# Kernel tuning notes

Hardware: AMD Instinct MI355X
Metric: run time of the kernel (lower is better)

The kernel has to match this reference:

```python
import jax, jax.numpy as jnp
import numpy as np

K = 2
N_NODES = 100_000
N_EDGES = 1_600_000
STATIC_F = 16
DYN_F = 32
EDGE_F = 8
IN_F = EDGE_F + 2 * STATIC_F + 2 * DYN_F  # 104
HID_F = 2 * DYN_F  # 64


def setup_inputs() -> dict:
    key = jax.random.key(0)
    ks = jax.random.split(key, 9)
    x_s = jax.random.normal(ks[0], (N_NODES, STATIC_F), dtype=jnp.float32)
    x_t = jax.random.normal(ks[1], (N_NODES, DYN_F), dtype=jnp.float32)
    edge_index = jax.random.randint(ks[2], (2, N_EDGES), 0, N_NODES, dtype=jnp.int64 if jax.config.jax_enable_x64 else jnp.int32)
    edge_attr = jax.random.normal(ks[3], (N_EDGES, EDGE_F), dtype=jnp.float32)
    W1 = jax.random.normal(ks[4], (IN_F, HID_F), dtype=jnp.float32) / np.sqrt(IN_F)
    b1 = jnp.zeros((HID_F,), dtype=jnp.float32)
    W2 = jax.random.normal(ks[5], (HID_F, DYN_F), dtype=jnp.float32) / np.sqrt(HID_F)
    b2 = jnp.zeros((DYN_F,), dtype=jnp.float32)
    F = jax.random.normal(ks[6], (K + 1, DYN_F, DYN_F), dtype=jnp.float32) / np.sqrt(DYN_F)
    return {"x_s": x_s, "x_t": x_t, "edge_index": edge_index, "edge_attr": edge_attr,
            "W1": W1, "b1": b1, "W2": W2, "b2": b2, "F": F}


def reference(x_s, x_t, edge_index, edge_attr, W1, b1, W2, b2, F):
    row, col = edge_index[0], edge_index[1]
    num_nodes = x_t.shape[0]
    # filter_matrix[0] (Linear, no bias); F[k] stored as [in, out]
    out = x_t @ F[0]
    xs_row = x_s[row]  # static gathers are loop-invariant
    xs_col = x_s[col]
    for k in range(K):
        mask = jnp.sum(out, axis=1) != 0  # [N]
        edge_mask = (mask[row] | mask[col]).astype(out.dtype)[:, None]  # [E,1]
        out_row = out[row]
        out_col = out[col]
        e_ij = jnp.concatenate([xs_row, xs_col, out_row, out_col, edge_attr], axis=1)  # [E,104]
        w_ij = jax.nn.relu(e_ij @ W1 + b1) @ W2 + b2  # [E,32]
        # normalize per edge; NaN (zero-norm) -> 0, matching masked_fill_
        nrm = jnp.linalg.norm(w_ij, axis=1, keepdims=True)
        w_ij = jnp.where(nrm > 0, w_ij / jnp.where(nrm > 0, nrm, 1.0), 0.0)
        # with_gradient: (x_j - x_i) * w_ij; zero out edges failing the mask
        shift = (out_col - out_row) * w_ij * edge_mask
        scattered = jax.ops.segment_sum(shift, col, num_segments=num_nodes)
        out = out + scattered @ F[k + 1]
    return out
```

## Files before the change

kernel.cpp:

```cpp
#include <hip/hip_runtime.h>

#define NN 100000
#define NE 1600000
#define SF 16
#define DF 32
#define EFT 8
#define HF 64

typedef __attribute__((ext_vector_type(8))) _Float16 half8;
typedef __attribute__((ext_vector_type(4))) _Float16 half4;
typedef __attribute__((ext_vector_type(8))) short short8;
typedef __attribute__((ext_vector_type(4))) float floatx4;

__global__ __launch_bounds__(256) void hist_kernel(const int* __restrict__ ei,
                                                   int* __restrict__ deg) {
  int e = blockIdx.x * 256 + threadIdx.x;
  if (e < NE) atomicAdd(&deg[ei[NE + e]], 1);
}

__global__ __launch_bounds__(256) void scan1_kernel(const int* __restrict__ deg,
                                                    int* __restrict__ cur,
                                                    int* __restrict__ bsums) {
  __shared__ int ts[256];
  int tid = threadIdx.x;
  int base = blockIdx.x * 1024 + tid * 4;
  int v[4];
#pragma unroll
  for (int q = 0; q < 4; ++q) v[q] = (base + q < NN) ? deg[base + q] : 0;
  int s = v[0] + v[1] + v[2] + v[3];
  ts[tid] = s;
  __syncthreads();
  for (int off = 1; off < 256; off <<= 1) {
    int t = (tid >= off) ? ts[tid - off] : 0;
    __syncthreads();
    ts[tid] += t;
    __syncthreads();
  }
  int excl = ts[tid] - s;
  if (tid == 255) bsums[blockIdx.x] = ts[255];
  int run = excl;
#pragma unroll
  for (int q = 0; q < 4; ++q) {
    if (base + q < NN) cur[base + q] = run;
    run += v[q];
  }
}

__global__ __launch_bounds__(256) void scan3_kernel(int* __restrict__ cur,
                                                    const int* __restrict__ bsums) {
  int i = blockIdx.x * 256 + threadIdx.x;
  int g = blockIdx.x >> 2;
  int pref = 0;
  for (int q = 0; q < g; ++q) pref += bsums[q];
  if (i < NN) cur[i] += pref;
}

__global__ __launch_bounds__(256) void setup_kernel(
    const float* __restrict__ W1, const float* __restrict__ W2,
    _Float16* __restrict__ WpreT, _Float16* __restrict__ w2pk,
    _Float16* __restrict__ w1epk,
    float4* __restrict__ scattered4, int* __restrict__ deg) {
  int gid = blockIdx.x * 256 + threadIdx.x;
  if (gid < 800000) {
    float4 z = {0.f, 0.f, 0.f, 0.f};
    scattered4[gid] = z;
  }
  if (gid < NN) deg[gid] = 0;
  if (gid < 128 * 64) {
    int col = gid >> 6, k = gid & 63;
    int j = col & 63;
    bool bh = col >= 64;
    float v = 0.f;
    if (k < 16) v = W1[((bh ? 16 : 0) + k) * HF + j];
    else if (k < 48) v = W1[((bh ? 64 : 32) + (k - 16)) * HF + j];
    WpreT[gid] = (_Float16)v;
  }
  if (gid < 2048) {
    int lane = gid >> 5, idx = gid & 31;
    int kt = idx >> 4, nt = (idx >> 3) & 1, q = idx & 7;
    int kgrp = (lane >> 4) & 3, lcol = lane & 15;
    w2pk[gid] = (_Float16)W2[(kt * 32 + kgrp * 8 + q) * DF + nt * 16 + lcol];
  } else if (gid < 4096) {
    int id = gid - 2048;
    int lane = id >> 5, idx = id & 31;
    int nt = idx >> 3, j = idx & 7;
    int lcol = lane & 15;
    float v = (lane < 16) ? W1[(96 + j) * HF + nt * 16 + lcol] : 0.f;
    w1epk[id] = (_Float16)v;
  }
}

__global__ __launch_bounds__(256) void fill_kernel(
    const int* __restrict__ ei, const float* __restrict__ ea,
    int* __restrict__ cur, int* __restrict__ row_s, int* __restrict__ col_s,
    _Float16* __restrict__ ea_s) {
  int e = blockIdx.x * 256 + threadIdx.x;
  int r = ei[e];
  int c = ei[NE + e];
  int pos = atomicAdd(&cur[c], 1);
  row_s[pos] = r;
  col_s[pos] = c;
  const float4* p = (const float4*)(ea + (size_t)e * EFT);
  float4 v0 = p[0], v1 = p[1];
  half8 h;
  h[0]=(_Float16)v0.x; h[1]=(_Float16)v0.y; h[2]=(_Float16)v0.z; h[3]=(_Float16)v0.w;
  h[4]=(_Float16)v1.x; h[5]=(_Float16)v1.y; h[6]=(_Float16)v1.z; h[7]=(_Float16)v1.w;
  *(half8*)(ea_s + (size_t)pos * 8) = h;
}

__global__ __launch_bounds__(256) void init_kernel(
    const float* __restrict__ x_t, const float* __restrict__ F0,
    float* __restrict__ out, _Float16* __restrict__ outb,
    float* __restrict__ sums) {
  int n = blockIdx.x * 256 + threadIdx.x;
  if (n >= NN) return;
  float x[DF];
  const float4* xr = reinterpret_cast<const float4*>(x_t + (size_t)n * DF);
#pragma unroll
  for (int q = 0; q < 8; ++q) {
    float4 v = xr[q];
    x[4*q+0]=v.x; x[4*q+1]=v.y; x[4*q+2]=v.z; x[4*q+3]=v.w;
  }
  float4* orow = reinterpret_cast<float4*>(out + (size_t)n * DF);
  _Float16* ob = outb + (size_t)n * DF;
  float s = 0.f;
#pragma unroll
  for (int q = 0; q < 8; ++q) {
    float4 acc = {0.f, 0.f, 0.f, 0.f};
#pragma unroll
    for (int i = 0; i < DF; ++i) {
      float xi = x[i];
      acc.x = fmaf(xi, F0[i*DF + 4*q+0], acc.x);
      acc.y = fmaf(xi, F0[i*DF + 4*q+1], acc.y);
      acc.z = fmaf(xi, F0[i*DF + 4*q+2], acc.z);
      acc.w = fmaf(xi, F0[i*DF + 4*q+3], acc.w);
    }
    orow[q] = acc;
    s += acc.x + acc.y + acc.z + acc.w;
    half4 pk = {(_Float16)acc.x, (_Float16)acc.y, (_Float16)acc.z, (_Float16)acc.w};
    *(half4*)(ob + 4*q) = pk;
  }
  sums[n] = s;
}

__global__ __launch_bounds__(256, 4) void pre_kernel(
    const float* __restrict__ x_s, const _Float16* __restrict__ outb,
    const _Float16* __restrict__ WpreT, _Float16* __restrict__ ABh) {
  __shared__ _Float16 wlds[128][72];
  int tid = threadIdx.x;
  for (int t = tid; t < 1024; t += 256) {
    int colr = t >> 3, kc = t & 7;
    *(half8*)(&wlds[colr][kc * 8]) = *(const half8*)(WpreT + colr * 64 + kc * 8);
  }
  __syncthreads();

  int lcol = tid & 15, kgrp = (tid >> 4) & 3, wid = tid >> 6;
  int nodebase = blockIdx.x * 64 + wid * 16;
  int nodeA = nodebase + lcol;

  half8 a0 = {}, a1 = {};
  if (nodeA < NN) {
    const _Float16* obp = outb + (size_t)nodeA * DF;
    if (kgrp < 2) {
      const float4* p = (const float4*)(x_s + (size_t)nodeA * SF);
      float4 v0 = p[kgrp * 2], v1 = p[kgrp * 2 + 1];
      a0[0]=(_Float16)v0.x; a0[1]=(_Float16)v0.y;
      a0[2]=(_Float16)v0.z; a0[3]=(_Float16)v0.w;
      a0[4]=(_Float16)v1.x; a0[5]=(_Float16)v1.y;
      a0[6]=(_Float16)v1.z; a0[7]=(_Float16)v1.w;
      a1 = *(const half8*)(obp + 16 + kgrp * 8);
    } else if (kgrp == 2) {
      a0 = *(const half8*)(obp + 0);
    } else {
      a0 = *(const half8*)(obp + 8);
    }
  }

  floatx4 acc[8];
#pragma unroll
  for (int nt = 0; nt < 8; ++nt) {
    half8 b0 = *(const half8*)(&wlds[nt * 16 + lcol][kgrp * 8]);
    half8 b1v = *(const half8*)(&wlds[nt * 16 + lcol][32 + kgrp * 8]);
    floatx4 c = {0.f, 0.f, 0.f, 0.f};
    c = __builtin_amdgcn_mfma_f32_16x16x32_f16(a0, b0, c, 0, 0, 0);
    c = __builtin_amdgcn_mfma_f32_16x16x32_f16(a1, b1v, c, 0, 0, 0);
    acc[nt] = c;
  }

#pragma unroll
  for (int rr = 0; rr < 4; ++rr) {
    int node = nodebase + kgrp * 4 + rr;
    if (node < NN) {
      _Float16* dst = ABh + (size_t)node * 128;
#pragma unroll
      for (int nt = 0; nt < 8; ++nt)
        dst[nt * 16 + lcol] = (_Float16)acc[nt][rr];
    }
  }
}

__global__ __launch_bounds__(256, 4) void edge_kernel(
    const _Float16* __restrict__ ABh, const _Float16* __restrict__ outb,
    const float* __restrict__ sums, const _Float16* __restrict__ ea_s,
    const int* __restrict__ row_s, const int* __restrict__ col_s,
    const float* __restrict__ b1, const float* __restrict__ b2,
    const _Float16* __restrict__ w2pk, const _Float16* __restrict__ w1epk,
    float* __restrict__ scattered) {
  __shared__ union { _Float16 h[256][72]; float sh[256][33]; } u;
  __shared__ int scol[256];
  __shared__ int srow[256];
  __shared__ union { float msk[256]; struct { unsigned short l0[256], l1[256]; } seg; } vv;
  __shared__ int wbase[4];
  __shared__ int cnt;

  int tid = threadIdx.x;
  int bbase = blockIdx.x * 256;
  int i = bbase + tid;
  if (tid == 0) cnt = 0;
  int lcol = tid & 15, kgrp = (tid >> 4) & 3, wid = tid >> 6;
  int lane = tid & 63;

  const _Float16* wpp = w2pk + (size_t)lane * 32;
  half8 w2f00 = *(const half8*)(wpp);
  half8 w2f01 = *(const half8*)(wpp + 8);
  half8 w2f10 = *(const half8*)(wpp + 16);
  half8 w2f11 = *(const half8*)(wpp + 24);
  float b2c0 = b2[lcol], b2c1 = b2[16 + lcol];

  int r = row_s[i];
  int c = col_s[i];
  scol[tid] = c;
  srow[tid] = r;
  float s_r = sums[r], s_c = sums[c];
  vv.msk[tid] = (s_r == 0.f && s_c == 0.f) ? 0.f : 1.f;

  half8 eav = *(const half8*)(ea_s + (size_t)i * 8);
  const _Float16* wep = w1epk + (size_t)lane * 32;
  half8 we0 = *(const half8*)(wep);
  half8 we1 = *(const half8*)(wep + 8);
  half8 we2 = *(const half8*)(wep + 16);
  half8 we3 = *(const half8*)(wep + 24);
  float b1c[4] = {b1[lcol], b1[16 + lcol], b1[32 + lcol], b1[48 + lcol]};
  int4 eai = __builtin_bit_cast(int4, eav);
  bool lo16 = lane < 16;
  int rbase0 = wid * 64 + kgrp * 4;
#pragma unroll
  for (int g = 0; g < 4; ++g) {
    int src = g * 16 + lcol;
    int4 t;
    t.x = __shfl(eai.x, src, 64);
    t.y = __shfl(eai.y, src, 64);
    t.z = __shfl(eai.z, src, 64);
    t.w = __shfl(eai.w, src, 64);
    half8 zz = {};
    half8 ag = lo16 ? __builtin_bit_cast(half8, t) : zz;
#pragma unroll
    for (int nt = 0; nt < 4; ++nt) {
      floatx4 cc = {b1c[nt], b1c[nt], b1c[nt], b1c[nt]};
      half8 wb = (nt == 0) ? we0 : (nt == 1) ? we1 : (nt == 2) ? we2 : we3;
      cc = __builtin_amdgcn_mfma_f32_16x16x32_f16(ag, wb, cc, 0, 0, 0);
      int rb = rbase0 + g * 16;
#pragma unroll
      for (int rr = 0; rr < 4; ++rr)
        u.h[rb + rr][nt * 16 + lcol] = (_Float16)cc[rr];
    }
  }
  __syncthreads();

  const _Float16* ar = ABh + (size_t)r * 128;
  const _Float16* bc = ABh + (size_t)c * 128 + 64;
#pragma unroll 4
  for (int q = 0; q < 8; ++q) {
    half8 a = *(const half8*)(ar + q * 8);
    half8 b = *(const half8*)(bc + q * 8);
    half8 w = *(const half8*)(&u.h[tid][q * 8]);
    half8 s = a + b + w;
    short8 sb = __builtin_bit_cast(short8, s);
    short8 m = sb >> 15;
    sb = sb & ~m;
    *(short8*)(&u.h[tid][q * 8]) = sb;
  }
  __syncthreads();

  floatx4 acc[4][2];
#pragma unroll
  for (int g = 0; g < 4; ++g) {
    int erow = wid * 64 + g * 16 + lcol;
    half8 a0 = *(const half8*)(&u.h[erow][kgrp * 8]);
    half8 a1 = *(const half8*)(&u.h[erow][32 + kgrp * 8]);
    floatx4 c0 = {b2c0, b2c0, b2c0, b2c0};
    floatx4 c1 = {b2c1, b2c1, b2c1, b2c1};
    c0 = __builtin_amdgcn_mfma_f32_16x16x32_f16(a0, w2f00, c0, 0, 0, 0);
    c0 = __builtin_amdgcn_mfma_f32_16x16x32_f16(a1, w2f10, c0, 0, 0, 0);
    c1 = __builtin_amdgcn_mfma_f32_16x16x32_f16(a0, w2f01, c1, 0, 0, 0);
    c1 = __builtin_amdgcn_mfma_f32_16x16x32_f16(a1, w2f11, c1, 0, 0, 0);
    acc[g][0] = c0;
    acc[g][1] = c1;
  }
  __syncthreads();

#pragma unroll
  for (int g = 0; g < 4; ++g) {
    float nsq[4];
#pragma unroll
    for (int rr = 0; rr < 4; ++rr)
      nsq[rr] = acc[g][0][rr]*acc[g][0][rr] + acc[g][1][rr]*acc[g][1][rr];
#pragma unroll
    for (int mm = 1; mm <= 8; mm <<= 1) {
#pragma unroll
      for (int rr = 0; rr < 4; ++rr)
        nsq[rr] += __shfl_xor(nsq[rr], mm, 64);
    }
#pragma unroll
    for (int rr = 0; rr < 4; ++rr) {
      int e = wid * 64 + g * 16 + kgrp * 4 + rr;
      float ms = (nsq[rr] > 0.f) ? rsqrtf(nsq[rr]) : 0.f;
      ms *= vv.msk[e];
      int r2 = srow[e];
      int c2 = scol[e];
      float ar0 = (float)outb[(size_t)r2 * DF + lcol];
      float ar1 = (float)outb[(size_t)r2 * DF + 16 + lcol];
      float bc0 = (float)outb[(size_t)c2 * DF + lcol];
      float bc1 = (float)outb[(size_t)c2 * DF + 16 + lcol];
      u.sh[e][lcol]      = (bc0 - ar0) * acc[g][0][rr] * ms;
      u.sh[e][16 + lcol] = (bc1 - ar1) * acc[g][1][rr] * ms;
    }
  }
  __syncthreads();

  int c_self = scol[tid];
  bool head = (tid == 0 || scol[tid - 1] != c_self);
  unsigned long long m = __ballot(head);
  if (lane == 0) wbase[wid] = atomicAdd(&cnt, (int)__popcll(m));
  __syncthreads();
  if (head) {
    int idx = wbase[wid] + (int)__popcll(m & ((1ull << lane) - 1ull));
    int t1 = tid + 1;
    while (t1 < 256 && scol[t1] == c_self) ++t1;
    vv.seg.l0[idx] = (unsigned short)tid;
    vv.seg.l1[idx] = (unsigned short)t1;
  }
  __syncthreads();
  int nr = cnt;
  for (int task = tid; task < nr * 32; task += 256) {
    int rid = task >> 5, j = task & 31;
    int t0 = vv.seg.l0[rid], t1 = vv.seg.l1[rid];
    float s = 0.f;
    for (int t = t0; t < t1; ++t) s += u.sh[t][j];
    unsafeAtomicAdd(&scattered[(size_t)scol[t0] * DF + j], s);
  }
}

__global__ __launch_bounds__(256) void node_kernel(
    float* __restrict__ out, float* __restrict__ scattered,
    const float* __restrict__ Fk, _Float16* __restrict__ outb,
    float* __restrict__ sums) {
  int n = blockIdx.x * 256 + threadIdx.x;
  if (n >= NN) return;
  float s[DF];
  float4* sp = reinterpret_cast<float4*>(scattered + (size_t)n * DF);
#pragma unroll
  for (int q = 0; q < 8; ++q) {
    float4 v = sp[q];
    s[4*q+0]=v.x; s[4*q+1]=v.y; s[4*q+2]=v.z; s[4*q+3]=v.w;
  }
  float4* op = reinterpret_cast<float4*>(out + (size_t)n * DF);
  _Float16* ob = outb + (size_t)n * DF;
  float ssum = 0.f;
#pragma unroll
  for (int q = 0; q < 8; ++q) {
    float4 acc = op[q];
#pragma unroll
    for (int i = 0; i < DF; ++i) {
      float si = s[i];
      acc.x = fmaf(si, Fk[i*DF + 4*q+0], acc.x);
      acc.y = fmaf(si, Fk[i*DF + 4*q+1], acc.y);
      acc.z = fmaf(si, Fk[i*DF + 4*q+2], acc.z);
      acc.w = fmaf(si, Fk[i*DF + 4*q+3], acc.w);
    }
    op[q] = acc;
    ssum += acc.x + acc.y + acc.z + acc.w;
    half4 pk = {(_Float16)acc.x, (_Float16)acc.y, (_Float16)acc.z, (_Float16)acc.w};
    *(half4*)(ob + 4*q) = pk;
  }
  sums[n] = ssum;
  float4 z = {0.f, 0.f, 0.f, 0.f};
#pragma unroll
  for (int q = 0; q < 8; ++q) sp[q] = z;
}

extern "C" void kernel_launch(void* const* d_in, const int* in_sizes, int n_in,
                              void* d_out, int out_size, void* d_ws, size_t ws_size,
                              hipStream_t stream) {
  const float* x_s = (const float*)d_in[0];
  const float* x_t = (const float*)d_in[1];
  const int*   ei  = (const int*)d_in[2];
  const float* ea  = (const float*)d_in[3];
  const float* W1  = (const float*)d_in[4];
  const float* b1  = (const float*)d_in[5];
  const float* W2  = (const float*)d_in[6];
  const float* b2  = (const float*)d_in[7];
  const float* F   = (const float*)d_in[8];

  float* out = (float*)d_out;
  char* ws = (char*)d_ws;
  float*     scattered = (float*)(ws);
  _Float16*  ABh       = (_Float16*)(ws + 12800000);
  _Float16*  outb      = (_Float16*)(ws + 38400000);
  float*     sums      = (float*)(ws + 44800000);
  int*       row_s     = (int*)(ws + 45200000);
  int*       col_s     = (int*)(ws + 51600000);
  int*       deg       = (int*)(ws + 58000000);
  int*       cur       = (int*)(ws + 58400000);
  int*       bsums     = (int*)(ws + 58800000);
  _Float16*  WpreT     = (_Float16*)(ws + 58810000);
  _Float16*  w2pk      = (_Float16*)(ws + 58830000);
  _Float16*  w1epk     = (_Float16*)(ws + 58840000);
  _Float16*  ea_s      = (_Float16*)(ws + 58900000);

  dim3 blk(256);
  dim3 grid_e(NE / 256);
  dim3 grid_n((NN + 255) / 256);
  dim3 grid_p((NN + 63) / 64);
  int nscan = (NN + 1023) / 1024;

  setup_kernel<<<3125, blk, 0, stream>>>(W1, W2, WpreT, w2pk, w1epk,
                                         (float4*)scattered, deg);
  hist_kernel<<<grid_e, blk, 0, stream>>>(ei, deg);
  scan1_kernel<<<nscan, blk, 0, stream>>>(deg, cur, bsums);
  scan3_kernel<<<grid_n, blk, 0, stream>>>(cur, bsums);
  fill_kernel<<<grid_e, blk, 0, stream>>>(ei, ea, cur, row_s, col_s, ea_s);

  init_kernel<<<grid_n, blk, 0, stream>>>(x_t, F, out, outb, sums);

  for (int k = 0; k < 2; ++k) {
    pre_kernel<<<grid_p, blk, 0, stream>>>(x_s, outb, WpreT, ABh);
    edge_kernel<<<grid_e, blk, 0, stream>>>(ABh, outb, sums, ea_s,
                                            row_s, col_s, b1, b2,
                                            w2pk, w1epk, scattered);
    node_kernel<<<grid_n, blk, 0, stream>>>(out, scattered,
                                            F + (size_t)(k + 1) * DF * DF,
                                            outb, sums);
  }
}
```

Measured before the change: 452.3 us.

## Pack edge records, transpose edge-attr MFMA, and per-thread normalize in edge kernel

Row, col and fp16 edge attributes are packed into one 24-byte record per sorted edge, so the edge kernel does a single contiguous load instead of three separate streams. The edge-attribute MFMA swaps its operands so each lane writes a contiguous half4 to its own edge row, which removes a __syncthreads before the gather stage. Normalization and the masked shift now run per thread over one edge, with vectorized half8 loads of outb, replacing cross-lane shuffle reductions and scalar gathers. Removing a barrier is only safe if every lane writes only its own LDS rows, and the per-thread 32-float staging adds register pressure.

New measurement: 451.1 us. No clear change (-0.3%).

```diff
diff --git a/kernel.cpp b/kernel.cpp
--- a/kernel.cpp
+++ b/kernel.cpp
@@ -8,7 +8,7 @@
 #define HF 64
 
 typedef __attribute__((ext_vector_type(8))) _Float16 half8;
-typedef __attribute__((ext_vector_type(4))) _Float16 half4;
+typedef __attribute__((ext_vector_type(4))) _Float16 half4v;
 typedef __attribute__((ext_vector_type(8))) short short8;
 typedef __attribute__((ext_vector_type(4))) float floatx4;
 
@@ -83,29 +83,31 @@
   } else if (gid < 4096) {
     int id = gid - 2048;
     int lane = id >> 5, idx = id & 31;
-    int nt = idx >> 3, j = idx & 7;
-    int lcol = lane & 15;
-    float v = (lane < 16) ? W1[(96 + j) * HF + nt * 16 + lcol] : 0.f;
+    int jblk = idx >> 3, t = idx & 7;
+    float v = (lane < 16) ? W1[(96 + t) * HF + jblk * 16 + lane] : 0.f;
     w1epk[id] = (_Float16)v;
   }
 }
 
 __global__ __launch_bounds__(256) void fill_kernel(
     const int* __restrict__ ei, const float* __restrict__ ea,
-    int* __restrict__ cur, int* __restrict__ row_s, int* __restrict__ col_s,
-    _Float16* __restrict__ ea_s) {
+    int* __restrict__ cur, char* __restrict__ recs) {
   int e = blockIdx.x * 256 + threadIdx.x;
   int r = ei[e];
   int c = ei[NE + e];
   int pos = atomicAdd(&cur[c], 1);
-  row_s[pos] = r;
-  col_s[pos] = c;
   const float4* p = (const float4*)(ea + (size_t)e * EFT);
   float4 v0 = p[0], v1 = p[1];
-  half8 h;
-  h[0]=(_Float16)v0.x; h[1]=(_Float16)v0.y; h[2]=(_Float16)v0.z; h[3]=(_Float16)v0.w;
-  h[4]=(_Float16)v1.x; h[5]=(_Float16)v1.y; h[6]=(_Float16)v1.z; h[7]=(_Float16)v1.w;
-  *(half8*)(ea_s + (size_t)pos * 8) = h;
+  union { _Float16 h[2]; int i; } p01, p23, p45, p67;
+  p01.h[0] = (_Float16)v0.x; p01.h[1] = (_Float16)v0.y;
+  p23.h[0] = (_Float16)v0.z; p23.h[1] = (_Float16)v0.w;
+  p45.h[0] = (_Float16)v1.x; p45.h[1] = (_Float16)v1.y;
+  p67.h[0] = (_Float16)v1.z; p67.h[1] = (_Float16)v1.w;
+  int2* rp = (int2*)(recs + (size_t)pos * 24);
+  int2 a = {r, c};
+  int2 b = {p01.i, p23.i};
+  int2 d = {p45.i, p67.i};
+  rp[0] = a; rp[1] = b; rp[2] = d;
 }
 
 __global__ __launch_bounds__(256) void init_kernel(
@@ -137,8 +139,8 @@
     }
     orow[q] = acc;
     s += acc.x + acc.y + acc.z + acc.w;
-    half4 pk = {(_Float16)acc.x, (_Float16)acc.y, (_Float16)acc.z, (_Float16)acc.w};
-    *(half4*)(ob + 4*q) = pk;
+    half4v pk = {(_Float16)acc.x, (_Float16)acc.y, (_Float16)acc.z, (_Float16)acc.w};
+    *(half4v*)(ob + 4*q) = pk;
   }
   sums[n] = s;
 }
@@ -201,15 +203,13 @@
 
 __global__ __launch_bounds__(256, 4) void edge_kernel(
     const _Float16* __restrict__ ABh, const _Float16* __restrict__ outb,
-    const float* __restrict__ sums, const _Float16* __restrict__ ea_s,
-    const int* __restrict__ row_s, const int* __restrict__ col_s,
+    const float* __restrict__ sums, const char* __restrict__ recs,
     const float* __restrict__ b1, const float* __restrict__ b2,
     const _Float16* __restrict__ w2pk, const _Float16* __restrict__ w1epk,
     float* __restrict__ scattered) {
-  __shared__ union { _Float16 h[256][72]; float sh[256][33]; } u;
+  __shared__ union { _Float16 h[256][72]; float sh[9472]; } u;
   __shared__ int scol[256];
-  __shared__ int srow[256];
-  __shared__ union { float msk[256]; struct { unsigned short l0[256], l1[256]; } seg; } vv;
+  __shared__ unsigned short l0[256], l1[256];
   __shared__ int wbase[4];
   __shared__ int cnt;
 
@@ -220,6 +220,14 @@
   int lcol = tid & 15, kgrp = (tid >> 4) & 3, wid = tid >> 6;
   int lane = tid & 63;
 
+  const int2* rp = (const int2*)(recs + (size_t)i * 24);
+  int2 ra = rp[0], rb = rp[1], rd = rp[2];
+  int r = ra.x;
+  int c = ra.y;
+  int4 eai = {rb.x, rb.y, rd.x, rd.y};
+  scol[tid] = c;
+  float s_r = sums[r], s_c = sums[c];
+
   const _Float16* wpp = w2pk + (size_t)lane * 32;
   half8 w2f00 = *(const half8*)(wpp);
   half8 w2f01 = *(const half8*)(wpp + 8);
@@ -227,23 +235,17 @@
   half8 w2f11 = *(const half8*)(wpp + 24);
   float b2c0 = b2[lcol], b2c1 = b2[16 + lcol];
 
-  int r = row_s[i];
-  int c = col_s[i];
-  scol[tid] = c;
-  srow[tid] = r;
-  float s_r = sums[r], s_c = sums[c];
-  vv.msk[tid] = (s_r == 0.f && s_c == 0.f) ? 0.f : 1.f;
-
-  half8 eav = *(const half8*)(ea_s + (size_t)i * 8);
   const _Float16* wep = w1epk + (size_t)lane * 32;
-  half8 we0 = *(const half8*)(wep);
-  half8 we1 = *(const half8*)(wep + 8);
-  half8 we2 = *(const half8*)(wep + 16);
-  half8 we3 = *(const half8*)(wep + 24);
-  float b1c[4] = {b1[lcol], b1[16 + lcol], b1[32 + lcol], b1[48 + lcol]};
-  int4 eai = __builtin_bit_cast(int4, eav);
+  half8 wA0 = *(const half8*)(wep);
+  half8 wA1 = *(const half8*)(wep + 8);
+  half8 wA2 = *(const half8*)(wep + 16);
+  half8 wA3 = *(const half8*)(wep + 24);
+  const float4* b1f4 = (const float4*)b1;
+  float4 b1q0 = b1f4[0 + kgrp];
+  float4 b1q1 = b1f4[4 + kgrp];
+  float4 b1q2 = b1f4[8 + kgrp];
+  float4 b1q3 = b1f4[12 + kgrp];
   bool lo16 = lane < 16;
-  int rbase0 = wid * 64 + kgrp * 4;
 #pragma unroll
   for (int g = 0; g < 4; ++g) {
     int src = g * 16 + lcol;
@@ -253,19 +255,34 @@
     t.z = __shfl(eai.z, src, 64);
     t.w = __shfl(eai.w, src, 64);
     half8 zz = {};
-    half8 ag = lo16 ? __builtin_bit_cast(half8, t) : zz;
-#pragma unroll
-    for (int nt = 0; nt < 4; ++nt) {
-      floatx4 cc = {b1c[nt], b1c[nt], b1c[nt], b1c[nt]};
-      half8 wb = (nt == 0) ? we0 : (nt == 1) ? we1 : (nt == 2) ? we2 : we3;
-      cc = __builtin_amdgcn_mfma_f32_16x16x32_f16(ag, wb, cc, 0, 0, 0);
-      int rb = rbase0 + g * 16;
-#pragma unroll
-      for (int rr = 0; rr < 4; ++rr)
-        u.h[rb + rr][nt * 16 + lcol] = (_Float16)cc[rr];
-    }
-  }
-  __syncthreads();
+    half8 bg = lo16 ? __builtin_bit_cast(half8, t) : zz;
+    int erow = wid * 64 + g * 16 + lcol;
+    _Float16* hrow = &u.h[erow][kgrp * 4];
+    {
+      floatx4 cc = {b1q0.x, b1q0.y, b1q0.z, b1q0.w};
+      cc = __builtin_amdgcn_mfma_f32_16x16x32_f16(wA0, bg, cc, 0, 0, 0);
+      half4v h4 = {(_Float16)cc[0], (_Float16)cc[1], (_Float16)cc[2], (_Float16)cc[3]};
+      *(half4v*)(hrow + 0) = h4;
+    }
+    {
+      floatx4 cc = {b1q1.x, b1q1.y, b1q1.z, b1q1.w};
+      cc = __builtin_amdgcn_mfma_f32_16x16x32_f16(wA1, bg, cc, 0, 0, 0);
+      half4v h4 = {(_Float16)cc[0], (_Float16)cc[1], (_Float16)cc[2], (_Float16)cc[3]};
+      *(half4v*)(hrow + 16) = h4;
+    }
+    {
+      floatx4 cc = {b1q2.x, b1q2.y, b1q2.z, b1q2.w};
+      cc = __builtin_amdgcn_mfma_f32_16x16x32_f16(wA2, bg, cc, 0, 0, 0);
+      half4v h4 = {(_Float16)cc[0], (_Float16)cc[1], (_Float16)cc[2], (_Float16)cc[3]};
+      *(half4v*)(hrow + 32) = h4;
+    }
+    {
+      floatx4 cc = {b1q3.x, b1q3.y, b1q3.z, b1q3.w};
+      cc = __builtin_amdgcn_mfma_f32_16x16x32_f16(wA3, bg, cc, 0, 0, 0);
+      half4v h4 = {(_Float16)cc[0], (_Float16)cc[1], (_Float16)cc[2], (_Float16)cc[3]};
+      *(half4v*)(hrow + 48) = h4;
+    }
+  }
 
   const _Float16* ar = ABh + (size_t)r * 128;
   const _Float16* bc = ABh + (size_t)c * 128 + 64;
@@ -280,7 +297,6 @@
     sb = sb & ~m;
     *(short8*)(&u.h[tid][q * 8]) = sb;
   }
-  __syncthreads();
 
   floatx4 acc[4][2];
 #pragma unroll
@@ -297,33 +313,39 @@
     acc[g][0] = c0;
     acc[g][1] = c1;
   }
+
   __syncthreads();
 
 #pragma unroll
   for (int g = 0; g < 4; ++g) {
-    float nsq[4];
-#pragma unroll
-    for (int rr = 0; rr < 4; ++rr)
-      nsq[rr] = acc[g][0][rr]*acc[g][0][rr] + acc[g][1][rr]*acc[g][1][rr];
-#pragma unroll
-    for (int mm = 1; mm <= 8; mm <<= 1) {
-#pragma unroll
-      for (int rr = 0; rr < 4; ++rr)
-        nsq[rr] += __shfl_xor(nsq[rr], mm, 64);
-    }
 #pragma unroll
     for (int rr = 0; rr < 4; ++rr) {
       int e = wid * 64 + g * 16 + kgrp * 4 + rr;
-      float ms = (nsq[rr] > 0.f) ? rsqrtf(nsq[rr]) : 0.f;
-      ms *= vv.msk[e];
-      int r2 = srow[e];
-      int c2 = scol[e];
-      float ar0 = (float)outb[(size_t)r2 * DF + lcol];
-      float ar1 = (float)outb[(size_t)r2 * DF + 16 + lcol];
-      float bc0 = (float)outb[(size_t)c2 * DF + lcol];
-      float bc1 = (float)outb[(size_t)c2 * DF + 16 + lcol];
-      u.sh[e][lcol]      = (bc0 - ar0) * acc[g][0][rr] * ms;
-      u.sh[e][16 + lcol] = (bc1 - ar1) * acc[g][1][rr] * ms;
+      u.sh[e * 37 + lcol]      = acc[g][0][rr];
+      u.sh[e * 37 + 16 + lcol] = acc[g][1][rr];
+    }
+  }
+
+  {
+    float o2[32];
+    float nsq = 0.f;
+#pragma unroll
+    for (int j = 0; j < 32; ++j) {
+      float v = u.sh[tid * 37 + j];
+      o2[j] = v;
+      nsq = fmaf(v, v, nsq);
+    }
+    float ms = (nsq > 0.f) ? rsqrtf(nsq) : 0.f;
+    if (s_r == 0.f && s_c == 0.f) ms = 0.f;
+    const half8* orp = (const half8*)(outb + (size_t)r * DF);
+    const half8* ocp = (const half8*)(outb + (size_t)c * DF);
+#pragma unroll
+    for (int q = 0; q < 4; ++q) {
+      half8 av = orp[q], bv = ocp[q];
+#pragma unroll
+      for (int jj = 0; jj < 8; ++jj)
+        u.sh[tid * 37 + q * 8 + jj] =
+            ((float)bv[jj] - (float)av[jj]) * o2[q * 8 + jj] * ms;
     }
   }
   __syncthreads();
@@ -337,16 +359,16 @@
     int idx = wbase[wid] + (int)__popcll(m & ((1ull << lane) - 1ull));
     int t1 = tid + 1;
     while (t1 < 256 && scol[t1] == c_self) ++t1;
-    vv.seg.l0[idx] = (unsigned short)tid;
-    vv.seg.l1[idx] = (unsigned short)t1;
+    l0[idx] = (unsigned short)tid;
+    l1[idx] = (unsigned short)t1;
   }
   __syncthreads();
   int nr = cnt;
   for (int task = tid; task < nr * 32; task += 256) {
     int rid = task >> 5, j = task & 31;
-    int t0 = vv.seg.l0[rid], t1 = vv.seg.l1[rid];
+    int t0 = l0[rid], t1 = l1[rid];
     float s = 0.f;
-    for (int t = t0; t < t1; ++t) s += u.sh[t][j];
+    for (int t = t0; t < t1; ++t) s += u.sh[t * 37 + j];
     unsafeAtomicAdd(&scattered[(size_t)scol[t0] * DF + j], s);
   }
 }
@@ -380,8 +402,8 @@
     }
     op[q] = acc;
     ssum += acc.x + acc.y + acc.z + acc.w;
-    half4 pk = {(_Float16)acc.x, (_Float16)acc.y, (_Float16)acc.z, (_Float16)acc.w};
-    *(half4*)(ob + 4*q) = pk;
+    half4v pk = {(_Float16)acc.x, (_Float16)acc.y, (_Float16)acc.z, (_Float16)acc.w};
+    *(half4v*)(ob + 4*q) = pk;
   }
   sums[n] = ssum;
   float4 z = {0.f, 0.f, 0.f, 0.f};
@@ -408,15 +430,13 @@
   _Float16*  ABh       = (_Float16*)(ws + 12800000);
   _Float16*  outb      = (_Float16*)(ws + 38400000);
   float*     sums      = (float*)(ws + 44800000);
-  int*       row_s     = (int*)(ws + 45200000);
-  int*       col_s     = (int*)(ws + 51600000);
-  int*       deg       = (int*)(ws + 58000000);
-  int*       cur       = (int*)(ws + 58400000);
-  int*       bsums     = (int*)(ws + 58800000);
-  _Float16*  WpreT     = (_Float16*)(ws + 58810000);
-  _Float16*  w2pk      = (_Float16*)(ws + 58830000);
-  _Float16*  w1epk     = (_Float16*)(ws + 58840000);
-  _Float16*  ea_s      = (_Float16*)(ws + 58900000);
+  char*      recs      = (char*)(ws + 45200000);
+  int*       deg       = (int*)(ws + 83600000);
+  int*       cur       = (int*)(ws + 84000000);
+  int*       bsums     = (int*)(ws + 84400000);
+  _Float16*  WpreT     = (_Float16*)(ws + 84410000);
+  _Float16*  w2pk      = (_Float16*)(ws + 84430000);
+  _Float16*  w1epk     = (_Float16*)(ws + 84440000);
 
   dim3 blk(256);
   dim3 grid_e(NE / 256);
@@ -429,14 +449,13 @@
   hist_kernel<<<grid_e, blk, 0, stream>>>(ei, deg);
   scan1_kernel<<<nscan, blk, 0, stream>>>(deg, cur, bsums);
   scan3_kernel<<<grid_n, blk, 0, stream>>>(cur, bsums);
-  fill_kernel<<<grid_e, blk, 0, stream>>>(ei, ea, cur, row_s, col_s, ea_s);
+  fill_kernel<<<grid_e, blk, 0, stream>>>(ei, ea, cur, recs);
 
   init_kernel<<<grid_n, blk, 0, stream>>>(x_t, F, out, outb, sums);
 
   for (int k = 0; k < 2; ++k) {
     pre_kernel<<<grid_p, blk, 0, stream>>>(x_s, outb, WpreT, ABh);
-    edge_kernel<<<grid_e, blk, 0, stream>>>(ABh, outb, sums, ea_s,
-                                            row_s, col_s, b1, b2,
+    edge_kernel<<<grid_e, blk, 0, stream>>>(ABh, outb, sums, recs, b1, b2,
                                             w2pk, w1epk, scattered);
     node_kernel<<<grid_n, blk, 0, stream>>>(out, scattered,
                                             F + (size_t)(k + 1) * DF * DF,
```
